# Optimization experiments

Measured on AMD Instinct MI355X. Metric: run time of the kernel, lower is better.

Reference implementation:

```python
import jax, jax.numpy as jnp
import numpy as np

EPS = 1e-5  # torch.nn.CosineSimilarity eps


def setup_inputs() -> dict:
    key = jax.random.key(0)
    x = jax.random.normal(key, (8, 256, 1024), dtype=jnp.float32)
    return {"batch_sequence_tensors": x}


def _worst_sim(x):
    # For every contiguous window [s, e] (1 <= s < e <= S-1, matching
    # exclude_special_tokens + sequential combinatorics), compute
    # min_t in [s,e] cos(mean(x[s:e+1]), x[t]).
    # Trick: dot(sum_{s..e} x_i, x_t) comes from a prefix sum of the Gram
    # matrix, and ||sum_{s..e} x||^2 from a 2-D prefix sum of the Gram matrix,
    # avoiding any [B,S,S,D] intermediates.
    B, S, D = x.shape
    G = jnp.einsum('bsd,btd->bst', x, x)  # [B,S,S] Gram

    # num[b,s,e,t] = sum_{i=s..e} x_i . x_t  via 1-D prefix sum over i
    Cpad = jnp.pad(jnp.cumsum(G, axis=1), ((0, 0), (1, 0), (0, 0)))  # [B,S+1,S]
    num = Cpad[:, 1:, :][:, None, :, :] - Cpad[:, :S, :][:, :, None, :]  # [B,S,S,S]

    # ||sum_{s..e} x||^2 = sum_{i,j in [s,e]} G[i,j] via 2-D prefix sum
    PP = jnp.pad(jnp.cumsum(jnp.cumsum(G, axis=1), axis=2),
                 ((0, 0), (1, 0), (1, 0)))  # [B,S+1,S+1]
    dE = jnp.diagonal(PP[:, 1:, 1:], axis1=1, axis2=2)   # PP[e+1,e+1]  [B,S]
    dS = jnp.diagonal(PP[:, :S, :S], axis1=1, axis2=2)   # PP[s,s]      [B,S]
    cross1 = PP[:, :S, 1:]                               # PP[s,e+1]  axes (s,e)
    cross2 = jnp.swapaxes(PP[:, 1:, :S], 1, 2)           # PP[e+1,s] -> (s,e)
    ssq = dE[:, None, :] + dS[:, :, None] - cross1 - cross2  # [B,S,S]
    sum_norm = jnp.sqrt(jnp.maximum(ssq, 0.0))               # ||sum||

    idx = jnp.arange(S)
    win_len = jnp.maximum(idx[None, :] - idx[:, None] + 1, 1).astype(x.dtype)  # [S,S] (s,e)
    # center = sum / len ; cosine uses the mean exactly as the torch module
    mean_norm = sum_norm / win_len                       # [B,S,S]
    x_norm = jnp.sqrt(jnp.maximum(jnp.diagonal(G, axis1=1, axis2=2), 0.0))  # [B,S]
    denom = jnp.maximum(mean_norm[..., None] * x_norm[:, None, None, :], EPS)
    cos = (num / win_len[None, :, :, None]) / denom      # [B,S,S,S]

    t_in = (idx[None, None, :] >= idx[:, None, None]) & \
           (idx[None, None, :] <= idx[None, :, None])    # [S,S,S] (s,e,t)
    worst = jnp.min(jnp.where(t_in[None], cos, jnp.inf), axis=-1)  # [B,S,S]

    valid = (idx[:, None] >= 1) & (idx[None, :] > idx[:, None])    # 1<=s<e<=S-1
    return jnp.where(valid[None], worst, 0.0)


def reference(batch_sequence_tensors):
    # worst_sim[b,s,e] = min cosine similarity of window mean vs members;
    # the original module's group mask is worst_sim >= threshold (0.9),
    # followed by (data-dependent, non-tensor) subset removal.
    return _worst_sim(batch_sequence_tensors)
```

## Files before the change

kernel.cpp:

```cpp
#include <hip/hip_runtime.h>
#include <stdint.h>

#define NB 8
#define NS 256
#define ND 1024
#define EPSF 1e-5f
#define BIGF 3.0e38f

typedef __attribute__((ext_vector_type(8))) short short8;
typedef __attribute__((ext_vector_type(4))) float f32x4;

__device__ __forceinline__ unsigned short f2bf(float f) {
  unsigned int u = __float_as_uint(f);
  u = (u + 0x7FFFu + ((u >> 16) & 1u)) >> 16;
  return (unsigned short)u;
}
__device__ __forceinline__ float bf2f(unsigned short u) {
  return __uint_as_float((unsigned int)u << 16);
}

__global__ __launch_bounds__(256) void k_convert(const float* __restrict__ x,
                                                 unsigned short* __restrict__ xb,
                                                 float* __restrict__ DGa,
                                                 float* __restrict__ IXa) {
  int row = blockIdx.x * 4 + (threadIdx.x >> 6);
  int lane = threadIdx.x & 63;
  size_t base = (size_t)row * ND;
  float sq = 0.f;
#pragma unroll
  for (int c = 0; c < 4; ++c) {
    size_t o = base + c * 256 + lane * 4;
    float4 v = *reinterpret_cast<const float4*>(x + o);
    ushort4 ob;
    ob.x = f2bf(v.x); ob.y = f2bf(v.y); ob.z = f2bf(v.z); ob.w = f2bf(v.w);
    *reinterpret_cast<ushort4*>(xb + o) = ob;
    sq += v.x * v.x + v.y * v.y + v.z * v.z + v.w * v.w;
  }
#pragma unroll
  for (int off = 32; off; off >>= 1) sq += __shfl_xor(sq, off);
  if (lane == 0) {
    DGa[row] = sq;
    IXa[row] = 1.0f / sqrtf(sq);
  }
}

__global__ __launch_bounds__(256) void k_ypfx(const unsigned short* __restrict__ xb,
                                              unsigned short* __restrict__ yb) {
  int gid = blockIdx.x * 256 + threadIdx.x;
  int b = gid >> 10;
  int d = gid & 1023;
  const unsigned short* xr = xb + ((size_t)b << 18) + d;
  unsigned short* yr = yb + ((size_t)b << 18) + d;
  float run = 0.f;
  for (int s = 0; s < NS; ++s) {
    run += bf2f(xr[(size_t)s * ND]);
    yr[(size_t)s * ND] = f2bf(run);
  }
}

__global__ __launch_bounds__(256) void k_gemmC(const unsigned short* __restrict__ yb,
                                               const unsigned short* __restrict__ xb,
                                               float* __restrict__ cp) {
  int gw = ((blockIdx.x << 8) + threadIdx.x) >> 6;
  int lane = threadIdx.x & 63;
  int b  = gw & 7;
  int mt = (gw >> 3) & 7;
  int nt = (gw >> 6) & 7;
  int ks = (gw >> 9) & 1;
  const unsigned short* Ab = yb + ((size_t)b << 18) + ((size_t)(mt << 5) << 10);
  const unsigned short* Bb = xb + ((size_t)b << 18) + ((size_t)(nt << 5) << 10);
  int lr = lane & 15;
  int lk = (lane >> 4) << 3;
  f32x4 acc00 = {0.f,0.f,0.f,0.f}, acc01 = {0.f,0.f,0.f,0.f};
  f32x4 acc10 = {0.f,0.f,0.f,0.f}, acc11 = {0.f,0.f,0.f,0.f};
  int kbase = (ks << 9) + lk;
#pragma unroll 2
  for (int kk = 0; kk < 512; kk += 32) {
    int ko = kbase + kk;
    short8 a0  = *reinterpret_cast<const short8*>(Ab + ((size_t)lr << 10) + ko);
    short8 a1  = *reinterpret_cast<const short8*>(Ab + ((size_t)(16 + lr) << 10) + ko);
    short8 bb0 = *reinterpret_cast<const short8*>(Bb + ((size_t)lr << 10) + ko);
    short8 bb1 = *reinterpret_cast<const short8*>(Bb + ((size_t)(16 + lr) << 10) + ko);
    acc00 = __builtin_amdgcn_mfma_f32_16x16x32_bf16(a0, bb0, acc00, 0, 0, 0);
    acc01 = __builtin_amdgcn_mfma_f32_16x16x32_bf16(a0, bb1, acc01, 0, 0, 0);
    acc10 = __builtin_amdgcn_mfma_f32_16x16x32_bf16(a1, bb0, acc10, 0, 0, 0);
    acc11 = __builtin_amdgcn_mfma_f32_16x16x32_bf16(a1, bb1, acc11, 0, 0, 0);
  }
  float* G = cp + (size_t)ks * (NB * NS * NS) + ((size_t)b << 16);
  int r0 = (mt << 5) + ((lane >> 4) << 2);
  int c0 = (nt << 5) + lr;
#pragma unroll
  for (int j = 0; j < 4; ++j) {
    G[(r0 + j) * NS + c0]           = acc00[j];
    G[(r0 + j) * NS + c0 + 16]      = acc01[j];
    G[(r0 + 16 + j) * NS + c0]      = acc10[j];
    G[(r0 + 16 + j) * NS + c0 + 16] = acc11[j];
  }
}

__global__ __launch_bounds__(256) void k_scan(const float* __restrict__ cp,
                                              float* __restrict__ C, float* __restrict__ S2) {
  int id = blockIdx.x * 4 + (threadIdx.x >> 6);
  int lane = threadIdx.x & 63;
  int b = id / 257;
  int r = id - b * 257;
  float* Crow = C + ((size_t)b * 257 + r) * NS;
  float* Srow = S2 + ((size_t)b * 257 + r) * 257;
  const float* p0 = cp + (((size_t)b << 8) + (r - 1)) * NS;
  const float* p1 = p0 + (size_t)NB * NS * NS;
  if (lane == 0) Srow[0] = 0.f;
  float run = 0.f;
  for (int c0 = 0; c0 < NS; c0 += 64) {
    float v = 0.f;
    if (r > 0) v = p0[c0 + lane] + p1[c0 + lane];
    Crow[c0 + lane] = v;
#pragma unroll
    for (int off = 1; off < 64; off <<= 1) {
      float n = __shfl_up(v, off);
      if (lane >= off) v += n;
    }
    Srow[c0 + lane + 1] = run + v;
    run += __shfl(v, 63);
  }
}

__global__ __launch_bounds__(256) void k_trop(const float* __restrict__ C,
                                              const float* __restrict__ S2,
                                              const float* __restrict__ IXa,
                                              const float* __restrict__ DGa,
                                              float* __restrict__ out) {
  __shared__ float As[64][36];
  __shared__ float Bs[64][68];
  __shared__ float wred[4];
  int blk = blockIdx.x;
  int b = blk >> 5;
  int tix = blk & 31;
  int i0 = (tix >> 2) << 5;
  int j0 = (tix & 3) << 6;
  int tid = threadIdx.x;
  float* outb = out + ((size_t)b << 16);

  if (i0 >= j0 + 63) {
    float4 z = {0.f, 0.f, 0.f, 0.f};
    float* p = outb + (size_t)(i0 + (tid >> 3)) * NS + j0 + ((tid & 7) << 3);
    reinterpret_cast<float4*>(p)[0] = z;
    reinterpret_cast<float4*>(p)[1] = z;
    return;
  }

  const float* Cb = C + (size_t)b * 257 * NS;
  const float* IXb = IXa + b * NS;

  float wv0 = IXb[tid];
#pragma unroll
  for (int off = 32; off; off >>= 1) wv0 = fmaxf(wv0, __shfl_xor(wv0, off));
  if ((tid & 63) == 0) wred[tid >> 6] = wv0;
  __syncthreads();
  float wmb = fmaxf(fmaxf(wred[0], wred[1]), fmaxf(wred[2], wred[3]));

  int ii0 = (tid >> 4) << 1;
  int jj0 = (tid & 15) << 2;
  float acc[8];
#pragma unroll
  for (int k = 0; k < 8; ++k) acc[k] = BIGF;

  int rA = tid >> 4;
  int c4 = (tid & 15) << 2;

  for (int t0 = i0 & ~63; t0 < j0 + 64; t0 += 64) {
    __syncthreads();
    float4 wv = *reinterpret_cast<const float4*>(IXb + t0 + c4);
#pragma unroll
    for (int p = 0; p < 2; ++p) {
      int r = i0 + p * 16 + rA;
      float4 v = *reinterpret_cast<const float4*>(Cb + (size_t)r * NS + t0 + c4);
      As[c4 + 0][p * 16 + rA] = v.x * wv.x;
      As[c4 + 1][p * 16 + rA] = v.y * wv.y;
      As[c4 + 2][p * 16 + rA] = v.z * wv.z;
      As[c4 + 3][p * 16 + rA] = v.w * wv.w;
    }
#pragma unroll
    for (int p = 0; p < 4; ++p) {
      int r = j0 + 1 + p * 16 + rA;
      float4 v = *reinterpret_cast<const float4*>(Cb + (size_t)r * NS + t0 + c4);
      Bs[c4 + 0][p * 16 + rA] = v.x * wv.x;
      Bs[c4 + 1][p * 16 + rA] = v.y * wv.y;
      Bs[c4 + 2][p * 16 + rA] = v.z * wv.z;
      Bs[c4 + 3][p * 16 + rA] = v.w * wv.w;
    }
    __syncthreads();

    int thA = i0 + ii0 - t0;
    int thB = j0 + jj0 - t0;
    if (thA <= -1 && thB >= 63) {
#pragma unroll 4
      for (int tt = 0; tt < 64; ++tt) {
        float2 a = *reinterpret_cast<const float2*>(&As[tt][ii0]);
        float4 bv = *reinterpret_cast<const float4*>(&Bs[tt][jj0]);
        acc[0] = fminf(acc[0], bv.x - a.x);
        acc[1] = fminf(acc[1], bv.y - a.x);
        acc[2] = fminf(acc[2], bv.z - a.x);
        acc[3] = fminf(acc[3], bv.w - a.x);
        acc[4] = fminf(acc[4], bv.x - a.y);
        acc[5] = fminf(acc[5], bv.y - a.y);
        acc[6] = fminf(acc[6], bv.z - a.y);
        acc[7] = fminf(acc[7], bv.w - a.y);
      }
    } else {
#pragma unroll 4
      for (int tt = 0; tt < 64; ++tt) {
        float2 a = *reinterpret_cast<const float2*>(&As[tt][ii0]);
        float4 bv = *reinterpret_cast<const float4*>(&Bs[tt][jj0]);
        float a0 = (tt >= thA)     ? a.x  : -BIGF;
        float a1 = (tt >= thA + 1) ? a.y  : -BIGF;
        float b0 = (tt <= thB)     ? bv.x :  BIGF;
        float b1 = (tt <= thB + 1) ? bv.y :  BIGF;
        float b2 = (tt <= thB + 2) ? bv.z :  BIGF;
        float b3 = (tt <= thB + 3) ? bv.w :  BIGF;
        acc[0] = fminf(acc[0], b0 - a0);
        acc[1] = fminf(acc[1], b1 - a0);
        acc[2] = fminf(acc[2], b2 - a0);
        acc[3] = fminf(acc[3], b3 - a0);
        acc[4] = fminf(acc[4], b0 - a1);
        acc[5] = fminf(acc[5], b1 - a1);
        acc[6] = fminf(acc[6], b2 - a1);
        acc[7] = fminf(acc[7], b3 - a1);
      }
    }
  }

  const float* S2b = S2 + (size_t)b * 257 * 257;
  const float* DGb = DGa + b * NS;
#pragma unroll
  for (int k = 0; k < 2; ++k) {
    int i = i0 + ii0 + k;
    float o4[4];
    float s2ii = S2b[(size_t)i * 257 + i];
#pragma unroll
    for (int l = 0; l < 4; ++l) {
      int j = j0 + jj0 + l;
      float res = 0.f;
      if (i >= 1 && j > i) {
        float s2jj = S2b[(size_t)(j + 1) * 257 + (j + 1)];
        float s2ij = S2b[(size_t)i * 257 + (j + 1)];
        float s2ji = S2b[(size_t)(j + 1) * 257 + i];
        float ssq = (s2jj - s2ij) - (s2ji - s2ii);
        float sn = sqrtf(fmaxf(ssq, 0.f));
        float win = (float)(j - i + 1);
        if (sn >= EPSF * win * wmb) {
          res = acc[k * 4 + l] / sn;
        } else {
          float mn = sn / win;
          float m = BIGF;
          const float* r2 = Cb + (size_t)(j + 1) * NS;
          const float* r1 = Cb + (size_t)i * NS;
          for (int t = i; t <= j; ++t) {
            float num = r2[t] - r1[t];
            float xn = sqrtf(fmaxf(DGb[t], 0.f));
            float den = fmaxf(mn * xn, EPSF);
            m = fminf(m, num / win / den);
          }
          res = m;
        }
      }
      o4[l] = res;
    }
    float4 st = {o4[0], o4[1], o4[2], o4[3]};
    *reinterpret_cast<float4*>(outb + (size_t)i * NS + j0 + jj0) = st;
  }
}

extern "C" void kernel_launch(void* const* d_in, const int* in_sizes, int n_in,
                              void* d_out, int out_size, void* d_ws, size_t ws_size,
                              hipStream_t stream) {
  (void)in_sizes; (void)n_in; (void)ws_size; (void)out_size;
  const float* x = (const float*)d_in[0];
  float* out = (float*)d_out;
  char* ws = (char*)d_ws;
  unsigned short* Xb = (unsigned short*)(ws);
  unsigned short* Yb = (unsigned short*)(ws + 4194304);
  float* Cp  = (float*)(ws + 8388608);
  float* C   = (float*)(ws + 12582912);
  float* S2  = (float*)(ws + 14688256);
  float* DGa = (float*)(ws + 16801824);
  float* IXa = (float*)(ws + 16810016);

  k_convert<<<512, 256, 0, stream>>>(x, Xb, DGa, IXa);
  k_ypfx<<<32, 256, 0, stream>>>(Xb, Yb);
  k_gemmC<<<256, 256, 0, stream>>>(Yb, Xb, Cp);
  k_scan<<<514, 256, 0, stream>>>(Cp, C, S2);
  k_trop<<<256, 256, 0, stream>>>(C, S2, IXa, DGa, out);
}
```

Baseline: 113.1 us.

## Fuse five-stage pipeline into one cooperative persistent kernel with grid syncs

Replaces the five separate kernel launches with a single cooperative kernel that runs each stage as a grid-stride loop separated by grid.sync(). The work is also re-tiled: the sequence prefix sum is now a parallel shared-memory scan read straight from fp32 input instead of a serial per-column loop, the GEMM uses 16x16 tiles per wave, and the tropical-min stage uses smaller 16x32 tiles. The aim is to remove launch overhead and raise parallelism in the low-occupancy stages. In exchange it adds grid-wide barrier costs and a host-side occupancy query on every launch.

New measurement: 314.2 us. 2.78x slower.

```diff
diff --git a/kernel.cpp b/kernel.cpp
--- a/kernel.cpp
+++ b/kernel.cpp
@@ -1,5 +1,8 @@
 #include <hip/hip_runtime.h>
+#include <hip/hip_cooperative_groups.h>
 #include <stdint.h>
+
+namespace cg = cooperative_groups;
 
 #define NB 8
 #define NS 256
@@ -15,258 +18,260 @@
   u = (u + 0x7FFFu + ((u >> 16) & 1u)) >> 16;
   return (unsigned short)u;
 }
-__device__ __forceinline__ float bf2f(unsigned short u) {
-  return __uint_as_float((unsigned int)u << 16);
-}
-
-__global__ __launch_bounds__(256) void k_convert(const float* __restrict__ x,
-                                                 unsigned short* __restrict__ xb,
-                                                 float* __restrict__ DGa,
-                                                 float* __restrict__ IXa) {
-  int row = blockIdx.x * 4 + (threadIdx.x >> 6);
-  int lane = threadIdx.x & 63;
-  size_t base = (size_t)row * ND;
-  float sq = 0.f;
-#pragma unroll
-  for (int c = 0; c < 4; ++c) {
-    size_t o = base + c * 256 + lane * 4;
-    float4 v = *reinterpret_cast<const float4*>(x + o);
+
+__global__ __launch_bounds__(256, 4) void k_fused(
+    const float* __restrict__ x, unsigned short* __restrict__ Xb,
+    unsigned short* __restrict__ Yb, float* __restrict__ Cp,
+    float* __restrict__ C, float* __restrict__ S2,
+    float* __restrict__ DGa, float* __restrict__ IXa,
+    float* __restrict__ out) {
+  __shared__ union {
+    struct { float xt[256][9]; float tot[8][33]; } p1;
+    struct { float As[64][17]; float Bs[64][34]; } p4;
+  } sm;
+  __shared__ float red[4];
+  cg::grid_group grid = cg::this_grid();
+
+  const int blk = blockIdx.x;
+  const int nblk = gridDim.x;
+  const int tid = threadIdx.x;
+  const int wv = tid >> 6;
+  const int lane = tid & 63;
+  const int nwave = nblk << 2;
+
+  for (int row = blk; row < NB * NS; row += nblk) {
+    float4 v = reinterpret_cast<const float4*>(x + (size_t)row * ND)[tid];
     ushort4 ob;
     ob.x = f2bf(v.x); ob.y = f2bf(v.y); ob.z = f2bf(v.z); ob.w = f2bf(v.w);
-    *reinterpret_cast<ushort4*>(xb + o) = ob;
-    sq += v.x * v.x + v.y * v.y + v.z * v.z + v.w * v.w;
-  }
-#pragma unroll
-  for (int off = 32; off; off >>= 1) sq += __shfl_xor(sq, off);
-  if (lane == 0) {
-    DGa[row] = sq;
-    IXa[row] = 1.0f / sqrtf(sq);
-  }
-}
-
-__global__ __launch_bounds__(256) void k_ypfx(const unsigned short* __restrict__ xb,
-                                              unsigned short* __restrict__ yb) {
-  int gid = blockIdx.x * 256 + threadIdx.x;
-  int b = gid >> 10;
-  int d = gid & 1023;
-  const unsigned short* xr = xb + ((size_t)b << 18) + d;
-  unsigned short* yr = yb + ((size_t)b << 18) + d;
-  float run = 0.f;
-  for (int s = 0; s < NS; ++s) {
-    run += bf2f(xr[(size_t)s * ND]);
-    yr[(size_t)s * ND] = f2bf(run);
-  }
-}
-
-__global__ __launch_bounds__(256) void k_gemmC(const unsigned short* __restrict__ yb,
-                                               const unsigned short* __restrict__ xb,
-                                               float* __restrict__ cp) {
-  int gw = ((blockIdx.x << 8) + threadIdx.x) >> 6;
-  int lane = threadIdx.x & 63;
-  int b  = gw & 7;
-  int mt = (gw >> 3) & 7;
-  int nt = (gw >> 6) & 7;
-  int ks = (gw >> 9) & 1;
-  const unsigned short* Ab = yb + ((size_t)b << 18) + ((size_t)(mt << 5) << 10);
-  const unsigned short* Bb = xb + ((size_t)b << 18) + ((size_t)(nt << 5) << 10);
-  int lr = lane & 15;
-  int lk = (lane >> 4) << 3;
-  f32x4 acc00 = {0.f,0.f,0.f,0.f}, acc01 = {0.f,0.f,0.f,0.f};
-  f32x4 acc10 = {0.f,0.f,0.f,0.f}, acc11 = {0.f,0.f,0.f,0.f};
-  int kbase = (ks << 9) + lk;
-#pragma unroll 2
-  for (int kk = 0; kk < 512; kk += 32) {
-    int ko = kbase + kk;
-    short8 a0  = *reinterpret_cast<const short8*>(Ab + ((size_t)lr << 10) + ko);
-    short8 a1  = *reinterpret_cast<const short8*>(Ab + ((size_t)(16 + lr) << 10) + ko);
-    short8 bb0 = *reinterpret_cast<const short8*>(Bb + ((size_t)lr << 10) + ko);
-    short8 bb1 = *reinterpret_cast<const short8*>(Bb + ((size_t)(16 + lr) << 10) + ko);
-    acc00 = __builtin_amdgcn_mfma_f32_16x16x32_bf16(a0, bb0, acc00, 0, 0, 0);
-    acc01 = __builtin_amdgcn_mfma_f32_16x16x32_bf16(a0, bb1, acc01, 0, 0, 0);
-    acc10 = __builtin_amdgcn_mfma_f32_16x16x32_bf16(a1, bb0, acc10, 0, 0, 0);
-    acc11 = __builtin_amdgcn_mfma_f32_16x16x32_bf16(a1, bb1, acc11, 0, 0, 0);
-  }
-  float* G = cp + (size_t)ks * (NB * NS * NS) + ((size_t)b << 16);
-  int r0 = (mt << 5) + ((lane >> 4) << 2);
-  int c0 = (nt << 5) + lr;
-#pragma unroll
-  for (int j = 0; j < 4; ++j) {
-    G[(r0 + j) * NS + c0]           = acc00[j];
-    G[(r0 + j) * NS + c0 + 16]      = acc01[j];
-    G[(r0 + 16 + j) * NS + c0]      = acc10[j];
-    G[(r0 + 16 + j) * NS + c0 + 16] = acc11[j];
-  }
-}
-
-__global__ __launch_bounds__(256) void k_scan(const float* __restrict__ cp,
-                                              float* __restrict__ C, float* __restrict__ S2) {
-  int id = blockIdx.x * 4 + (threadIdx.x >> 6);
-  int lane = threadIdx.x & 63;
-  int b = id / 257;
-  int r = id - b * 257;
-  float* Crow = C + ((size_t)b * 257 + r) * NS;
-  float* Srow = S2 + ((size_t)b * 257 + r) * 257;
-  const float* p0 = cp + (((size_t)b << 8) + (r - 1)) * NS;
-  const float* p1 = p0 + (size_t)NB * NS * NS;
-  if (lane == 0) Srow[0] = 0.f;
-  float run = 0.f;
-  for (int c0 = 0; c0 < NS; c0 += 64) {
-    float v = 0.f;
-    if (r > 0) v = p0[c0 + lane] + p1[c0 + lane];
-    Crow[c0 + lane] = v;
-#pragma unroll
-    for (int off = 1; off < 64; off <<= 1) {
-      float n = __shfl_up(v, off);
-      if (lane >= off) v += n;
-    }
-    Srow[c0 + lane + 1] = run + v;
-    run += __shfl(v, 63);
-  }
-}
-
-__global__ __launch_bounds__(256) void k_trop(const float* __restrict__ C,
-                                              const float* __restrict__ S2,
-                                              const float* __restrict__ IXa,
-                                              const float* __restrict__ DGa,
-                                              float* __restrict__ out) {
-  __shared__ float As[64][36];
-  __shared__ float Bs[64][68];
-  __shared__ float wred[4];
-  int blk = blockIdx.x;
-  int b = blk >> 5;
-  int tix = blk & 31;
-  int i0 = (tix >> 2) << 5;
-  int j0 = (tix & 3) << 6;
-  int tid = threadIdx.x;
-  float* outb = out + ((size_t)b << 16);
-
-  if (i0 >= j0 + 63) {
-    float4 z = {0.f, 0.f, 0.f, 0.f};
-    float* p = outb + (size_t)(i0 + (tid >> 3)) * NS + j0 + ((tid & 7) << 3);
-    reinterpret_cast<float4*>(p)[0] = z;
-    reinterpret_cast<float4*>(p)[1] = z;
-    return;
-  }
-
-  const float* Cb = C + (size_t)b * 257 * NS;
-  const float* IXb = IXa + b * NS;
-
-  float wv0 = IXb[tid];
-#pragma unroll
-  for (int off = 32; off; off >>= 1) wv0 = fmaxf(wv0, __shfl_xor(wv0, off));
-  if ((tid & 63) == 0) wred[tid >> 6] = wv0;
-  __syncthreads();
-  float wmb = fmaxf(fmaxf(wred[0], wred[1]), fmaxf(wred[2], wred[3]));
-
-  int ii0 = (tid >> 4) << 1;
-  int jj0 = (tid & 15) << 2;
-  float acc[8];
-#pragma unroll
-  for (int k = 0; k < 8; ++k) acc[k] = BIGF;
-
-  int rA = tid >> 4;
-  int c4 = (tid & 15) << 2;
-
-  for (int t0 = i0 & ~63; t0 < j0 + 64; t0 += 64) {
-    __syncthreads();
-    float4 wv = *reinterpret_cast<const float4*>(IXb + t0 + c4);
-#pragma unroll
-    for (int p = 0; p < 2; ++p) {
-      int r = i0 + p * 16 + rA;
-      float4 v = *reinterpret_cast<const float4*>(Cb + (size_t)r * NS + t0 + c4);
-      As[c4 + 0][p * 16 + rA] = v.x * wv.x;
-      As[c4 + 1][p * 16 + rA] = v.y * wv.y;
-      As[c4 + 2][p * 16 + rA] = v.z * wv.z;
-      As[c4 + 3][p * 16 + rA] = v.w * wv.w;
-    }
-#pragma unroll
-    for (int p = 0; p < 4; ++p) {
-      int r = j0 + 1 + p * 16 + rA;
-      float4 v = *reinterpret_cast<const float4*>(Cb + (size_t)r * NS + t0 + c4);
-      Bs[c4 + 0][p * 16 + rA] = v.x * wv.x;
-      Bs[c4 + 1][p * 16 + rA] = v.y * wv.y;
-      Bs[c4 + 2][p * 16 + rA] = v.z * wv.z;
-      Bs[c4 + 3][p * 16 + rA] = v.w * wv.w;
-    }
-    __syncthreads();
-
-    int thA = i0 + ii0 - t0;
-    int thB = j0 + jj0 - t0;
-    if (thA <= -1 && thB >= 63) {
+    reinterpret_cast<ushort4*>(Xb + (size_t)row * ND)[tid] = ob;
+    float sq = v.x * v.x + v.y * v.y + v.z * v.z + v.w * v.w;
+#pragma unroll
+    for (int off = 32; off; off >>= 1) sq += __shfl_xor(sq, off);
+    if (lane == 0) red[wv] = sq;
+    __syncthreads();
+    if (tid == 0) {
+      float s = red[0] + red[1] + red[2] + red[3];
+      DGa[row] = s;
+      IXa[row] = 1.0f / sqrtf(s);
+    }
+    __syncthreads();
+  }
+
+  for (int tile = blk; tile < 1024; tile += nblk) {
+    __syncthreads();
+    int b = tile >> 7;
+    int d0 = (tile & 127) << 3;
+    const float* xs = x + ((size_t)b << 18) + d0;
+#pragma unroll
+    for (int q = 0; q < 2; ++q) {
+      int slot = tid + (q << 8);
+      int s = slot >> 1, h = (slot & 1) << 2;
+      float4 v = *reinterpret_cast<const float4*>(xs + (size_t)s * ND + h);
+      sm.p1.xt[s][h + 0] = v.x;
+      sm.p1.xt[s][h + 1] = v.y;
+      sm.p1.xt[s][h + 2] = v.z;
+      sm.p1.xt[s][h + 3] = v.w;
+    }
+    __syncthreads();
+    int col = tid & 7, ch = tid >> 3;
+    float loc[8];
+    float run = 0.f;
+#pragma unroll
+    for (int r = 0; r < 8; ++r) { run += sm.p1.xt[ch * 8 + r][col]; loc[r] = run; }
+    sm.p1.tot[col][ch] = run;
+    __syncthreads();
+#pragma unroll
+    for (int off = 1; off < 32; off <<= 1) {
+      float tv = (ch >= off) ? sm.p1.tot[col][ch - off] : 0.f;
+      __syncthreads();
+      sm.p1.tot[col][ch] += tv;
+      __syncthreads();
+    }
+    float excl = sm.p1.tot[col][ch] - run;
+#pragma unroll
+    for (int r = 0; r < 8; ++r) sm.p1.xt[ch * 8 + r][col] = excl + loc[r];
+    __syncthreads();
+    unsigned short* yr = Yb + ((size_t)b << 18) + (size_t)tid * ND + d0;
+    ushort4 o0, o1;
+    o0.x = f2bf(sm.p1.xt[tid][0]); o0.y = f2bf(sm.p1.xt[tid][1]);
+    o0.z = f2bf(sm.p1.xt[tid][2]); o0.w = f2bf(sm.p1.xt[tid][3]);
+    o1.x = f2bf(sm.p1.xt[tid][4]); o1.y = f2bf(sm.p1.xt[tid][5]);
+    o1.z = f2bf(sm.p1.xt[tid][6]); o1.w = f2bf(sm.p1.xt[tid][7]);
+    reinterpret_cast<ushort4*>(yr)[0] = o0;
+    reinterpret_cast<ushort4*>(yr)[1] = o1;
+  }
+
+  grid.sync();
+
+  for (int job = (blk << 2) + wv; job < 4096; job += nwave) {
+    int b = job >> 9;
+    int r2 = job & 511;
+    int ks = r2 & 1;
+    int nt = (r2 >> 1) & 15;
+    int mt = r2 >> 5;
+    const unsigned short* Ab = Yb + ((size_t)b << 18) + ((size_t)(mt << 4) << 10);
+    const unsigned short* Bb = Xb + ((size_t)b << 18) + ((size_t)(nt << 4) << 10);
+    int lr = lane & 15;
+    int kbase = (ks << 9) + ((lane >> 4) << 3);
+    f32x4 ae = {0.f, 0.f, 0.f, 0.f}, ao = {0.f, 0.f, 0.f, 0.f};
 #pragma unroll 4
-      for (int tt = 0; tt < 64; ++tt) {
-        float2 a = *reinterpret_cast<const float2*>(&As[tt][ii0]);
-        float4 bv = *reinterpret_cast<const float4*>(&Bs[tt][jj0]);
-        acc[0] = fminf(acc[0], bv.x - a.x);
-        acc[1] = fminf(acc[1], bv.y - a.x);
-        acc[2] = fminf(acc[2], bv.z - a.x);
-        acc[3] = fminf(acc[3], bv.w - a.x);
-        acc[4] = fminf(acc[4], bv.x - a.y);
-        acc[5] = fminf(acc[5], bv.y - a.y);
-        acc[6] = fminf(acc[6], bv.z - a.y);
-        acc[7] = fminf(acc[7], bv.w - a.y);
+    for (int kk = 0; kk < 512; kk += 64) {
+      const unsigned short* ap = Ab + ((size_t)lr << 10) + kbase + kk;
+      const unsigned short* bp = Bb + ((size_t)lr << 10) + kbase + kk;
+      short8 a0 = *reinterpret_cast<const short8*>(ap);
+      short8 b0 = *reinterpret_cast<const short8*>(bp);
+      short8 a1 = *reinterpret_cast<const short8*>(ap + 32);
+      short8 b1 = *reinterpret_cast<const short8*>(bp + 32);
+      ae = __builtin_amdgcn_mfma_f32_16x16x32_bf16(a0, b0, ae, 0, 0, 0);
+      ao = __builtin_amdgcn_mfma_f32_16x16x32_bf16(a1, b1, ao, 0, 0, 0);
+    }
+    f32x4 acc = ae + ao;
+    float* P = Cp + (size_t)ks * (NB * NS * NS) + ((size_t)b << 16);
+    int r0 = (mt << 4) + ((lane >> 4) << 2);
+    int c0 = (nt << 4) + lr;
+#pragma unroll
+    for (int j = 0; j < 4; ++j) P[(size_t)(r0 + j) * NS + c0] = acc[j];
+  }
+
+  grid.sync();
+
+  for (int job = (blk << 2) + wv; job < NB * 257; job += nwave) {
+    int b = job / 257;
+    int r = job - b * 257;
+    float* Crow = C + ((size_t)b * 257 + r) * NS;
+    float* Srow = S2 + ((size_t)b * 257 + r) * 257;
+    int rm1 = (r > 0) ? (r - 1) : 0;
+    const float* p0 = Cp + (((size_t)b << 8) + rm1) * NS;
+    const float* p1 = p0 + (size_t)(NB * NS * NS);
+    if (lane == 0) Srow[0] = 0.f;
+    float run = 0.f;
+    for (int c0 = 0; c0 < NS; c0 += 64) {
+      float v = 0.f;
+      if (r > 0) v = p0[c0 + lane] + p1[c0 + lane];
+      Crow[c0 + lane] = v;
+#pragma unroll
+      for (int off = 1; off < 64; off <<= 1) {
+        float n = __shfl_up(v, off);
+        if (lane >= off) v += n;
       }
-    } else {
-#pragma unroll 4
-      for (int tt = 0; tt < 64; ++tt) {
-        float2 a = *reinterpret_cast<const float2*>(&As[tt][ii0]);
-        float4 bv = *reinterpret_cast<const float4*>(&Bs[tt][jj0]);
-        float a0 = (tt >= thA)     ? a.x  : -BIGF;
-        float a1 = (tt >= thA + 1) ? a.y  : -BIGF;
-        float b0 = (tt <= thB)     ? bv.x :  BIGF;
-        float b1 = (tt <= thB + 1) ? bv.y :  BIGF;
-        float b2 = (tt <= thB + 2) ? bv.z :  BIGF;
-        float b3 = (tt <= thB + 3) ? bv.w :  BIGF;
-        acc[0] = fminf(acc[0], b0 - a0);
-        acc[1] = fminf(acc[1], b1 - a0);
-        acc[2] = fminf(acc[2], b2 - a0);
-        acc[3] = fminf(acc[3], b3 - a0);
-        acc[4] = fminf(acc[4], b0 - a1);
-        acc[5] = fminf(acc[5], b1 - a1);
-        acc[6] = fminf(acc[6], b2 - a1);
-        acc[7] = fminf(acc[7], b3 - a1);
-      }
-    }
-  }
-
-  const float* S2b = S2 + (size_t)b * 257 * 257;
-  const float* DGb = DGa + b * NS;
-#pragma unroll
-  for (int k = 0; k < 2; ++k) {
-    int i = i0 + ii0 + k;
-    float o4[4];
-    float s2ii = S2b[(size_t)i * 257 + i];
-#pragma unroll
-    for (int l = 0; l < 4; ++l) {
-      int j = j0 + jj0 + l;
-      float res = 0.f;
-      if (i >= 1 && j > i) {
-        float s2jj = S2b[(size_t)(j + 1) * 257 + (j + 1)];
-        float s2ij = S2b[(size_t)i * 257 + (j + 1)];
-        float s2ji = S2b[(size_t)(j + 1) * 257 + i];
-        float ssq = (s2jj - s2ij) - (s2ji - s2ii);
-        float sn = sqrtf(fmaxf(ssq, 0.f));
-        float win = (float)(j - i + 1);
-        if (sn >= EPSF * win * wmb) {
-          res = acc[k * 4 + l] / sn;
+      Srow[c0 + lane + 1] = run + v;
+      run += __shfl(v, 63);
+    }
+  }
+
+  grid.sync();
+
+  for (int tile = blk; tile < 1024; tile += nblk) {
+    __syncthreads();
+    int b = tile >> 7;
+    int tix = tile & 127;
+    int i0 = (tix >> 3) << 4;
+    int j0 = (tix & 7) << 5;
+    float* outb = out + ((size_t)b << 16);
+
+    if (i0 > j0 + 30) {
+      float2 z = {0.f, 0.f};
+      *reinterpret_cast<float2*>(outb + (size_t)(i0 + (tid >> 4)) * NS + j0 + ((tid & 15) << 1)) = z;
+      continue;
+    }
+
+    const float* Cb = C + (size_t)b * 257 * NS;
+    const float* IXb = IXa + b * NS;
+    float w0 = IXb[tid];
+#pragma unroll
+    for (int off = 32; off; off >>= 1) w0 = fmaxf(w0, __shfl_xor(w0, off));
+    if (lane == 0) red[wv] = w0;
+    __syncthreads();
+    float wmb = fmaxf(fmaxf(red[0], red[1]), fmaxf(red[2], red[3]));
+
+    int ii = tid >> 4;
+    int jj = (tid & 15) << 1;
+    float acc0 = BIGF, acc1 = BIGF;
+
+    for (int t0 = i0 & ~63; t0 < j0 + 32; t0 += 64) {
+      __syncthreads();
+#pragma unroll
+      for (int q = 0; q < 3; ++q) {
+        int slot = tid + (q << 8);
+        int rrow = slot >> 4;
+        int c4 = (slot & 15) << 2;
+        float4 wv4 = *reinterpret_cast<const float4*>(IXb + t0 + c4);
+        if (rrow < 16) {
+          float4 v = *reinterpret_cast<const float4*>(Cb + (size_t)(i0 + rrow) * NS + t0 + c4);
+          sm.p4.As[c4 + 0][rrow] = v.x * wv4.x;
+          sm.p4.As[c4 + 1][rrow] = v.y * wv4.y;
+          sm.p4.As[c4 + 2][rrow] = v.z * wv4.z;
+          sm.p4.As[c4 + 3][rrow] = v.w * wv4.w;
         } else {
-          float mn = sn / win;
-          float m = BIGF;
-          const float* r2 = Cb + (size_t)(j + 1) * NS;
-          const float* r1 = Cb + (size_t)i * NS;
-          for (int t = i; t <= j; ++t) {
-            float num = r2[t] - r1[t];
-            float xn = sqrtf(fmaxf(DGb[t], 0.f));
-            float den = fmaxf(mn * xn, EPSF);
-            m = fminf(m, num / win / den);
-          }
-          res = m;
+          int rb = rrow - 16;
+          float4 v = *reinterpret_cast<const float4*>(Cb + (size_t)(j0 + 1 + rb) * NS + t0 + c4);
+          sm.p4.Bs[c4 + 0][rb] = v.x * wv4.x;
+          sm.p4.Bs[c4 + 1][rb] = v.y * wv4.y;
+          sm.p4.Bs[c4 + 2][rb] = v.z * wv4.z;
+          sm.p4.Bs[c4 + 3][rb] = v.w * wv4.w;
         }
       }
-      o4[l] = res;
-    }
-    float4 st = {o4[0], o4[1], o4[2], o4[3]};
-    *reinterpret_cast<float4*>(outb + (size_t)i * NS + j0 + jj0) = st;
+      __syncthreads();
+      int thA = i0 + ii - t0;
+      int thB = j0 + jj - t0;
+      if (thA <= 0 && thB >= 63) {
+#pragma unroll 8
+        for (int tt = 0; tt < 64; ++tt) {
+          float a = sm.p4.As[tt][ii];
+          float2 bv = *reinterpret_cast<const float2*>(&sm.p4.Bs[tt][jj]);
+          acc0 = fminf(acc0, bv.x - a);
+          acc1 = fminf(acc1, bv.y - a);
+        }
+      } else {
+#pragma unroll 8
+        for (int tt = 0; tt < 64; ++tt) {
+          float a = (tt >= thA) ? sm.p4.As[tt][ii] : -BIGF;
+          float2 bv = *reinterpret_cast<const float2*>(&sm.p4.Bs[tt][jj]);
+          float b0 = (tt <= thB) ? bv.x : BIGF;
+          float b1 = (tt <= thB + 1) ? bv.y : BIGF;
+          acc0 = fminf(acc0, b0 - a);
+          acc1 = fminf(acc1, b1 - a);
+        }
+      }
+    }
+
+    const float* S2b = S2 + (size_t)b * 257 * 257;
+    const float* DGb = DGa + b * NS;
+    int i = i0 + ii;
+    float res[2] = {0.f, 0.f};
+    if (i >= 1) {
+      float s2ii = S2b[(size_t)i * 257 + i];
+      float am[2] = {acc0, acc1};
+#pragma unroll
+      for (int l = 0; l < 2; ++l) {
+        int j = j0 + jj + l;
+        if (j > i) {
+          float s2jj = S2b[(size_t)(j + 1) * 257 + (j + 1)];
+          float s2ij = S2b[(size_t)i * 257 + (j + 1)];
+          float s2ji = S2b[(size_t)(j + 1) * 257 + i];
+          float ssq = (s2jj - s2ij) - (s2ji - s2ii);
+          float sn = sqrtf(fmaxf(ssq, 0.f));
+          float win = (float)(j - i + 1);
+          if (sn >= EPSF * win * wmb) {
+            res[l] = am[l] / sn;
+          } else {
+            float mn = sn / win;
+            float m = BIGF;
+            const float* r2p = Cb + (size_t)(j + 1) * NS;
+            const float* r1p = Cb + (size_t)i * NS;
+            for (int t = i; t <= j; ++t) {
+              float num = r2p[t] - r1p[t];
+              float xn = sqrtf(fmaxf(DGb[t], 0.f));
+              float den = fmaxf(mn * xn, EPSF);
+              m = fminf(m, num / win / den);
+            }
+            res[l] = m;
+          }
+        }
+      }
+    }
+    float2 st = {res[0], res[1]};
+    *reinterpret_cast<float2*>(outb + (size_t)i * NS + j0 + jj) = st;
   }
 }
 
@@ -285,9 +290,13 @@
   float* DGa = (float*)(ws + 16801824);
   float* IXa = (float*)(ws + 16810016);
 
-  k_convert<<<512, 256, 0, stream>>>(x, Xb, DGa, IXa);
-  k_ypfx<<<32, 256, 0, stream>>>(Xb, Yb);
-  k_gemmC<<<256, 256, 0, stream>>>(Yb, Xb, Cp);
-  k_scan<<<514, 256, 0, stream>>>(Cp, C, S2);
-  k_trop<<<256, 256, 0, stream>>>(C, S2, IXa, DGa, out);
+  int maxB = 0;
+  if (hipOccupancyMaxActiveBlocksPerMultiprocessor(&maxB, k_fused, 256, 0) != hipSuccess || maxB < 1)
+    maxB = 1;
+  long grid = (long)maxB * 256;
+  if (grid > 1024) grid = 1024;
+
+  void* args[] = {(void*)&x, (void*)&Xb, (void*)&Yb, (void*)&Cp, (void*)&C,
+                  (void*)&S2, (void*)&DGa, (void*)&IXa, (void*)&out};
+  hipLaunchCooperativeKernel((void*)k_fused, dim3((uint32_t)grid), dim3(256), args, 0, stream);
 }
```

## Fuse convert and prefix-sum kernels, drop split-K GEMM partials

Applied to the files above, without the earlier changes.

Merges the bf16 convert and the sequence prefix-sum into one launch. The prefix sum now runs as a parallel shared-memory scan over 8-column tiles read directly from fp32 input, replacing the old serial per-column loop that used 32 blocks. The GEMM drops split-K in favour of 16x16 tiles per wave over the full K. It writes straight into the C buffer at row offset 1, so the scan kernel no longer reads and adds two partial buffers. This removes a launch, the serial scan bottleneck and the partial-sum traffic, at the cost of more smaller GEMM jobs that reuse less data per wave.

Result: faster. 109.1 us (-3.5%).

```diff
diff --git a/kernel.cpp b/kernel.cpp
--- a/kernel.cpp
+++ b/kernel.cpp
@@ -15,105 +15,131 @@
   u = (u + 0x7FFFu + ((u >> 16) & 1u)) >> 16;
   return (unsigned short)u;
 }
-__device__ __forceinline__ float bf2f(unsigned short u) {
-  return __uint_as_float((unsigned int)u << 16);
-}
-
-__global__ __launch_bounds__(256) void k_convert(const float* __restrict__ x,
-                                                 unsigned short* __restrict__ xb,
-                                                 float* __restrict__ DGa,
-                                                 float* __restrict__ IXa) {
-  int row = blockIdx.x * 4 + (threadIdx.x >> 6);
-  int lane = threadIdx.x & 63;
-  size_t base = (size_t)row * ND;
-  float sq = 0.f;
-#pragma unroll
-  for (int c = 0; c < 4; ++c) {
-    size_t o = base + c * 256 + lane * 4;
-    float4 v = *reinterpret_cast<const float4*>(x + o);
-    ushort4 ob;
-    ob.x = f2bf(v.x); ob.y = f2bf(v.y); ob.z = f2bf(v.z); ob.w = f2bf(v.w);
-    *reinterpret_cast<ushort4*>(xb + o) = ob;
-    sq += v.x * v.x + v.y * v.y + v.z * v.z + v.w * v.w;
-  }
-#pragma unroll
-  for (int off = 32; off; off >>= 1) sq += __shfl_xor(sq, off);
-  if (lane == 0) {
-    DGa[row] = sq;
-    IXa[row] = 1.0f / sqrtf(sq);
-  }
-}
-
-__global__ __launch_bounds__(256) void k_ypfx(const unsigned short* __restrict__ xb,
-                                              unsigned short* __restrict__ yb) {
-  int gid = blockIdx.x * 256 + threadIdx.x;
-  int b = gid >> 10;
-  int d = gid & 1023;
-  const unsigned short* xr = xb + ((size_t)b << 18) + d;
-  unsigned short* yr = yb + ((size_t)b << 18) + d;
+
+__global__ __launch_bounds__(256) void k_pre(const float* __restrict__ x,
+                                             unsigned short* __restrict__ Xb,
+                                             unsigned short* __restrict__ Yb,
+                                             float* __restrict__ DGa,
+                                             float* __restrict__ IXa) {
+  __shared__ struct { float xt[256][9]; float tot[8][33]; } sm;
+  int blk = blockIdx.x;
+  int tid = threadIdx.x;
+  int lane = tid & 63;
+
+  if (blk < 512) {
+    int row = blk * 4 + (tid >> 6);
+    size_t base = (size_t)row * ND;
+    float sq = 0.f;
+#pragma unroll
+    for (int c = 0; c < 4; ++c) {
+      size_t o = base + c * 256 + lane * 4;
+      float4 v = *reinterpret_cast<const float4*>(x + o);
+      ushort4 ob;
+      ob.x = f2bf(v.x); ob.y = f2bf(v.y); ob.z = f2bf(v.z); ob.w = f2bf(v.w);
+      *reinterpret_cast<ushort4*>(Xb + o) = ob;
+      sq += v.x * v.x + v.y * v.y + v.z * v.z + v.w * v.w;
+    }
+#pragma unroll
+    for (int off = 32; off; off >>= 1) sq += __shfl_xor(sq, off);
+    if (lane == 0) {
+      DGa[row] = sq;
+      IXa[row] = 1.0f / sqrtf(sq);
+    }
+    return;
+  }
+
+  int tile = blk - 512;
+  int b = tile >> 7;
+  int d0 = (tile & 127) << 3;
+  const float* xs = x + ((size_t)b << 18) + d0;
+#pragma unroll
+  for (int q = 0; q < 2; ++q) {
+    int slot = tid + (q << 8);
+    int s = slot >> 1, h = (slot & 1) << 2;
+    float4 v = *reinterpret_cast<const float4*>(xs + (size_t)s * ND + h);
+    sm.xt[s][h + 0] = v.x;
+    sm.xt[s][h + 1] = v.y;
+    sm.xt[s][h + 2] = v.z;
+    sm.xt[s][h + 3] = v.w;
+  }
+  __syncthreads();
+  int col = tid & 7, ch = tid >> 3;
+  float loc[8];
   float run = 0.f;
-  for (int s = 0; s < NS; ++s) {
-    run += bf2f(xr[(size_t)s * ND]);
-    yr[(size_t)s * ND] = f2bf(run);
-  }
+#pragma unroll
+  for (int r = 0; r < 8; ++r) { run += sm.xt[ch * 8 + r][col]; loc[r] = run; }
+  sm.tot[col][ch] = run;
+  __syncthreads();
+#pragma unroll
+  for (int off = 1; off < 32; off <<= 1) {
+    float tv = (ch >= off) ? sm.tot[col][ch - off] : 0.f;
+    __syncthreads();
+    sm.tot[col][ch] += tv;
+    __syncthreads();
+  }
+  float excl = sm.tot[col][ch] - run;
+#pragma unroll
+  for (int r = 0; r < 8; ++r) sm.xt[ch * 8 + r][col] = excl + loc[r];
+  __syncthreads();
+  unsigned short* yr = Yb + ((size_t)b << 18) + (size_t)tid * ND + d0;
+  ushort4 o0, o1;
+  o0.x = f2bf(sm.xt[tid][0]); o0.y = f2bf(sm.xt[tid][1]);
+  o0.z = f2bf(sm.xt[tid][2]); o0.w = f2bf(sm.xt[tid][3]);
+  o1.x = f2bf(sm.xt[tid][4]); o1.y = f2bf(sm.xt[tid][5]);
+  o1.z = f2bf(sm.xt[tid][6]); o1.w = f2bf(sm.xt[tid][7]);
+  reinterpret_cast<ushort4*>(yr)[0] = o0;
+  reinterpret_cast<ushort4*>(yr)[1] = o1;
 }
 
 __global__ __launch_bounds__(256) void k_gemmC(const unsigned short* __restrict__ yb,
                                                const unsigned short* __restrict__ xb,
-                                               float* __restrict__ cp) {
-  int gw = ((blockIdx.x << 8) + threadIdx.x) >> 6;
+                                               float* __restrict__ C) {
+  int job = (blockIdx.x << 2) + (threadIdx.x >> 6);
   int lane = threadIdx.x & 63;
-  int b  = gw & 7;
-  int mt = (gw >> 3) & 7;
-  int nt = (gw >> 6) & 7;
-  int ks = (gw >> 9) & 1;
-  const unsigned short* Ab = yb + ((size_t)b << 18) + ((size_t)(mt << 5) << 10);
-  const unsigned short* Bb = xb + ((size_t)b << 18) + ((size_t)(nt << 5) << 10);
+  int b = job >> 8;
+  int mt = (job >> 4) & 15;
+  int nt = job & 15;
+  const unsigned short* Ab = yb + ((size_t)b << 18) + ((size_t)(mt << 4) << 10);
+  const unsigned short* Bb = xb + ((size_t)b << 18) + ((size_t)(nt << 4) << 10);
   int lr = lane & 15;
-  int lk = (lane >> 4) << 3;
-  f32x4 acc00 = {0.f,0.f,0.f,0.f}, acc01 = {0.f,0.f,0.f,0.f};
-  f32x4 acc10 = {0.f,0.f,0.f,0.f}, acc11 = {0.f,0.f,0.f,0.f};
-  int kbase = (ks << 9) + lk;
-#pragma unroll 2
-  for (int kk = 0; kk < 512; kk += 32) {
-    int ko = kbase + kk;
-    short8 a0  = *reinterpret_cast<const short8*>(Ab + ((size_t)lr << 10) + ko);
-    short8 a1  = *reinterpret_cast<const short8*>(Ab + ((size_t)(16 + lr) << 10) + ko);
-    short8 bb0 = *reinterpret_cast<const short8*>(Bb + ((size_t)lr << 10) + ko);
-    short8 bb1 = *reinterpret_cast<const short8*>(Bb + ((size_t)(16 + lr) << 10) + ko);
-    acc00 = __builtin_amdgcn_mfma_f32_16x16x32_bf16(a0, bb0, acc00, 0, 0, 0);
-    acc01 = __builtin_amdgcn_mfma_f32_16x16x32_bf16(a0, bb1, acc01, 0, 0, 0);
-    acc10 = __builtin_amdgcn_mfma_f32_16x16x32_bf16(a1, bb0, acc10, 0, 0, 0);
-    acc11 = __builtin_amdgcn_mfma_f32_16x16x32_bf16(a1, bb1, acc11, 0, 0, 0);
-  }
-  float* G = cp + (size_t)ks * (NB * NS * NS) + ((size_t)b << 16);
-  int r0 = (mt << 5) + ((lane >> 4) << 2);
-  int c0 = (nt << 5) + lr;
-#pragma unroll
-  for (int j = 0; j < 4; ++j) {
-    G[(r0 + j) * NS + c0]           = acc00[j];
-    G[(r0 + j) * NS + c0 + 16]      = acc01[j];
-    G[(r0 + 16 + j) * NS + c0]      = acc10[j];
-    G[(r0 + 16 + j) * NS + c0 + 16] = acc11[j];
-  }
-}
-
-__global__ __launch_bounds__(256) void k_scan(const float* __restrict__ cp,
-                                              float* __restrict__ C, float* __restrict__ S2) {
+  int kbase = (lane >> 4) << 3;
+  f32x4 ae = {0.f, 0.f, 0.f, 0.f}, ao = {0.f, 0.f, 0.f, 0.f};
+#pragma unroll 4
+  for (int kk = 0; kk < 1024; kk += 64) {
+    const unsigned short* ap = Ab + ((size_t)lr << 10) + kbase + kk;
+    const unsigned short* bp = Bb + ((size_t)lr << 10) + kbase + kk;
+    short8 a0 = *reinterpret_cast<const short8*>(ap);
+    short8 b0 = *reinterpret_cast<const short8*>(bp);
+    short8 a1 = *reinterpret_cast<const short8*>(ap + 32);
+    short8 b1 = *reinterpret_cast<const short8*>(bp + 32);
+    ae = __builtin_amdgcn_mfma_f32_16x16x32_bf16(a0, b0, ae, 0, 0, 0);
+    ao = __builtin_amdgcn_mfma_f32_16x16x32_bf16(a1, b1, ao, 0, 0, 0);
+  }
+  f32x4 acc = ae + ao;
+  float* Cb = C + (size_t)b * 257 * NS;
+  int r0 = (mt << 4) + ((lane >> 4) << 2) + 1;
+  int c0 = (nt << 4) + lr;
+#pragma unroll
+  for (int j = 0; j < 4; ++j) Cb[(size_t)(r0 + j) * NS + c0] = acc[j];
+}
+
+__global__ __launch_bounds__(256) void k_scan(float* __restrict__ C, float* __restrict__ S2) {
   int id = blockIdx.x * 4 + (threadIdx.x >> 6);
   int lane = threadIdx.x & 63;
   int b = id / 257;
   int r = id - b * 257;
   float* Crow = C + ((size_t)b * 257 + r) * NS;
   float* Srow = S2 + ((size_t)b * 257 + r) * 257;
-  const float* p0 = cp + (((size_t)b << 8) + (r - 1)) * NS;
-  const float* p1 = p0 + (size_t)NB * NS * NS;
   if (lane == 0) Srow[0] = 0.f;
   float run = 0.f;
   for (int c0 = 0; c0 < NS; c0 += 64) {
-    float v = 0.f;
-    if (r > 0) v = p0[c0 + lane] + p1[c0 + lane];
-    Crow[c0 + lane] = v;
+    float v;
+    if (r > 0) {
+      v = Crow[c0 + lane];
+    } else {
+      v = 0.f;
+      Crow[c0 + lane] = 0.f;
+    }
 #pragma unroll
     for (int off = 1; off < 64; off <<= 1) {
       float n = __shfl_up(v, off);
@@ -279,15 +305,13 @@
   char* ws = (char*)d_ws;
   unsigned short* Xb = (unsigned short*)(ws);
   unsigned short* Yb = (unsigned short*)(ws + 4194304);
-  float* Cp  = (float*)(ws + 8388608);
-  float* C   = (float*)(ws + 12582912);
-  float* S2  = (float*)(ws + 14688256);
-  float* DGa = (float*)(ws + 16801824);
-  float* IXa = (float*)(ws + 16810016);
-
-  k_convert<<<512, 256, 0, stream>>>(x, Xb, DGa, IXa);
-  k_ypfx<<<32, 256, 0, stream>>>(Xb, Yb);
-  k_gemmC<<<256, 256, 0, stream>>>(Yb, Xb, Cp);
-  k_scan<<<514, 256, 0, stream>>>(Cp, C, S2);
+  float* C   = (float*)(ws + 8388608);
+  float* S2  = (float*)(ws + 10493952);
+  float* DGa = (float*)(ws + 12607520);
+  float* IXa = (float*)(ws + 12615712);
+
+  k_pre<<<1536, 256, 0, stream>>>(x, Xb, Yb, DGa, IXa);
+  k_gemmC<<<512, 256, 0, stream>>>(Yb, Xb, C);
+  k_scan<<<514, 256, 0, stream>>>(C, S2);
   k_trop<<<256, 256, 0, stream>>>(C, S2, IXa, DGa, out);
 }
```
